# Kernel tuning notes

Hardware: AMD Instinct MI355X
Metric: run time of the kernel (lower is better)

## Reference

```python
import jax, jax.numpy as jnp
import numpy as np

N_NODES = 50000
N_EDGES = 800000
IN_F = 128
HID_F = 128
OUT_F = 128

def safediv(a, b):
    b = jnp.where(b == 0, jnp.ones_like(b), b)
    return a / b

def setup_inputs() -> dict:
    key = jax.random.key(0)
    ks = jax.random.split(key, 8)
    h = jax.random.normal(ks[0], (N_NODES, IN_F), dtype=jnp.float32)
    ppr_weight = jax.random.uniform(ks[1], (N_EDGES,), dtype=jnp.float32)
    Qw = jax.random.normal(ks[2], (HID_F, IN_F), dtype=jnp.float32) * (1.0 / np.sqrt(IN_F))
    Qb = jnp.zeros((HID_F,), dtype=jnp.float32)
    Ww = jax.random.normal(ks[3], (OUT_F, IN_F + HID_F), dtype=jnp.float32) * (1.0 / np.sqrt(IN_F + HID_F))
    Wb = jnp.zeros((OUT_F,), dtype=jnp.float32)
    src = jax.random.randint(ks[4], (N_EDGES,), 0, N_NODES, dtype=jnp.int64 if jax.config.jax_enable_x64 else jnp.int32)
    dst = jax.random.randint(ks[5], (N_EDGES,), 0, N_NODES, dtype=jnp.int64 if jax.config.jax_enable_x64 else jnp.int32)
    return {"h": h, "ppr_weight": ppr_weight, "Qw": Qw, "Qb": Qb, "Ww": Ww, "Wb": Wb, "src": src, "dst": dst}

def reference(h, ppr_weight, Qw, Qb, Ww, Wb, src, dst):
    # neighbor transform: Q(h) -> [N, HID_F]
    hq = h @ Qw.T + Qb
    # message: h_w = hq[src] * ppr_weight  (edge-weighted gather) [E, HID_F]
    msg = hq[src] * ppr_weight[:, None]
    # reduce: scatter-sum messages and weights onto dst nodes
    h_agg = jax.ops.segment_sum(msg, dst, num_segments=N_NODES)
    w = jax.ops.segment_sum(ppr_weight, dst, num_segments=N_NODES)
    # apply: PPR-weighted mean, concat, linear, leaky_relu, L2 normalize
    h_agg = safediv(h_agg, w[:, None])
    h_concat = jnp.concatenate([h, h_agg], axis=1)
    h_new = jax.nn.leaky_relu(h_concat @ Ww.T + Wb, negative_slope=0.01)
    norm = jnp.linalg.norm(h_new, axis=1, keepdims=True)
    return safediv(h_new, norm)
```

## Files before the change

### kernel.cpp

```cpp
#include <hip/hip_runtime.h>
#include <stdint.h>

#define N_NODES 50000
#define N_EDGES 800000
#define IN_F 128
#define HID_F 128
#define OUT_F 128
#define CAT_F 256
#define N_STRIPS 3125

#define NB 256
#define NBUCK 782
#define CHUNK_E (N_EDGES / NB)
#define BCAP 1280

typedef __bf16 bf16x8 __attribute__((ext_vector_type(8)));
typedef float f32x4 __attribute__((ext_vector_type(4)));

union BF8 {
  bf16x8 v;
  uint16_t u[8];
};

__device__ __forceinline__ uint32_t f2b(float f) {
  uint32_t u = __float_as_uint(f);
  return (u + 0x7fffu + ((u >> 16) & 1u)) >> 16;
}

__global__ void __launch_bounds__(256) prep_hist_kernel(
    const int* __restrict__ dst, int* __restrict__ G,
    const float* __restrict__ Qw, const float* __restrict__ Ww,
    uint16_t* __restrict__ QwB, uint16_t* __restrict__ WwB) {
  if (blockIdx.x < NB) {
    __shared__ int hist[NBUCK];
    for (int k = threadIdx.x; k < NBUCK; k += 256) hist[k] = 0;
    __syncthreads();
    int base = blockIdx.x * CHUNK_E;
    for (int e = base + threadIdx.x; e < base + CHUNK_E; e += 256)
      atomicAdd(&hist[dst[e] >> 6], 1);
    __syncthreads();
    for (int k = threadIdx.x; k < NBUCK; k += 256)
      G[k * NB + blockIdx.x] = hist[k];
  } else {
    const int TOT4 = (HID_F * IN_F + OUT_F * CAT_F) / 4;
    int i4 = (blockIdx.x - NB) * 256 + threadIdx.x;
    if (i4 >= TOT4) return;
    int base = i4 * 4;
    const float* src;
    uint16_t* dstp;
    int off;
    if (base < HID_F * IN_F) {
      src = Qw; dstp = QwB; off = base;
    } else {
      src = Ww; dstp = WwB; off = base - HID_F * IN_F;
    }
    float4 v = *(const float4*)(src + off);
    ushort4 o;
    o.x = (uint16_t)f2b(v.x); o.y = (uint16_t)f2b(v.y);
    o.z = (uint16_t)f2b(v.z); o.w = (uint16_t)f2b(v.w);
    *(ushort4*)(dstp + off) = o;
  }
}

__global__ void __launch_bounds__(256) bucket_scan_kernel(const int* __restrict__ G,
                                                          int* __restrict__ Gs,
                                                          int* __restrict__ Btot) {
  int w = (blockIdx.x * 256 + (int)threadIdx.x) >> 6;
  if (w >= NBUCK) return;
  int lane = threadIdx.x & 63;
  int4 v = *(const int4*)(G + (size_t)w * NB + lane * 4);
  int s = v.x + v.y + v.z + v.w;
  int inc = s;
#pragma unroll
  for (int d = 1; d < 64; d <<= 1) {
    int x = __shfl_up(inc, d, 64);
    if (lane >= d) inc += x;
  }
  int exc = inc - s;
  int4 o;
  o.x = exc;
  o.y = exc + v.x;
  o.z = exc + v.x + v.y;
  o.w = exc + v.x + v.y + v.z;
  *(int4*)(Gs + (size_t)w * NB + lane * 4) = o;
  if (lane == 63) Btot[w] = inc;
}

__global__ void base_scan_kernel(const int* __restrict__ Btot, int* __restrict__ Bbase) {
  int lane = threadIdx.x;
  int c[13], loc[13];
  int s = 0;
#pragma unroll
  for (int j = 0; j < 13; ++j) {
    int i = lane * 13 + j;
    c[j] = (i < NBUCK) ? Btot[i] : 0;
    loc[j] = s;
    s += c[j];
  }
  int inc = s;
#pragma unroll
  for (int d = 1; d < 64; d <<= 1) {
    int x = __shfl_up(inc, d, 64);
    if (lane >= d) inc += x;
  }
  int exc = inc - s;
#pragma unroll
  for (int j = 0; j < 13; ++j) {
    int i = lane * 13 + j;
    if (i <= NBUCK) Bbase[i] = exc + loc[j];
  }
}

__device__ __forceinline__ void gemm1_body(int gb, const float* __restrict__ h,
                                           const uint16_t* __restrict__ QwB,
                                           const float* __restrict__ Qb,
                                           uint16_t* __restrict__ hqB) {
  int wave = (gb * 256 + (int)threadIdx.x) >> 6;
  if (wave >= N_STRIPS) return;
  int lane = threadIdx.x & 63;
  int r = lane & 15, qd = lane >> 4;
  int row0 = wave * 16;
  f32x4 acc[8];
#pragma unroll
  for (int t = 0; t < 8; ++t) acc[t] = (f32x4){0.f, 0.f, 0.f, 0.f};
  const float* aRow = h + (size_t)(row0 + r) * IN_F + qd * 8;
#pragma unroll
  for (int kt = 0; kt < 4; ++kt) {
    float4 v0 = *(const float4*)(aRow + kt * 32);
    float4 v1 = *(const float4*)(aRow + kt * 32 + 4);
    BF8 a;
    a.u[0] = (uint16_t)f2b(v0.x); a.u[1] = (uint16_t)f2b(v0.y);
    a.u[2] = (uint16_t)f2b(v0.z); a.u[3] = (uint16_t)f2b(v0.w);
    a.u[4] = (uint16_t)f2b(v1.x); a.u[5] = (uint16_t)f2b(v1.y);
    a.u[6] = (uint16_t)f2b(v1.z); a.u[7] = (uint16_t)f2b(v1.w);
#pragma unroll
    for (int t = 0; t < 8; ++t) {
      bf16x8 b = *(const bf16x8*)(QwB + (t * 16 + r) * IN_F + kt * 32 + qd * 8);
      acc[t] = __builtin_amdgcn_mfma_f32_16x16x32_bf16(a.v, b, acc[t], 0, 0, 0);
    }
  }
#pragma unroll
  for (int t = 0; t < 8; ++t) {
    float qb = Qb[t * 16 + r];
#pragma unroll
    for (int rr = 0; rr < 4; ++rr) {
      int m = row0 + qd * 4 + rr;
      hqB[(size_t)m * HID_F + t * 16 + r] = (uint16_t)f2b(acc[t][rr] + qb);
    }
  }
}

__global__ void __launch_bounds__(256) scatter_gemm1_kernel(
    const int* __restrict__ dst, const int* __restrict__ src, const float* __restrict__ ppr,
    const int* __restrict__ Gs, const int* __restrict__ Bbase, int2* __restrict__ rec,
    const float* __restrict__ h, const uint16_t* __restrict__ QwB,
    const float* __restrict__ Qb, uint16_t* __restrict__ hqB) {
  if (blockIdx.x < NB) {
    __shared__ int cursor[NBUCK];
    int b = blockIdx.x;
    for (int k = threadIdx.x; k < NBUCK; k += 256)
      cursor[k] = Bbase[k] + Gs[(size_t)k * NB + b];
    __syncthreads();
    int base = b * CHUNK_E;
    for (int e = base + threadIdx.x; e < base + CHUNK_E; e += 256) {
      int d = dst[e];
      int s = src[e];
      float w = ppr[e];
      int pos = atomicAdd(&cursor[d >> 6], 1);
      rec[pos] = make_int2(s | ((d & 63) << 20), __float_as_int(w));
    }
  } else {
    gemm1_body(blockIdx.x - NB, h, QwB, Qb, hqB);
  }
}

__global__ void __launch_bounds__(256) agg_gemm2_kernel(
    const uint16_t* __restrict__ hqB, const int2* __restrict__ rec,
    const int* __restrict__ Bbase, const float* __restrict__ h,
    const uint16_t* __restrict__ WwB, const float* __restrict__ Wb,
    float* __restrict__ out) {
  __shared__ int2 srec[BCAP];
  __shared__ uint4 hagg[64][17];
  __shared__ int hist[64];
  __shared__ int noff[65];
  __shared__ int cur[64];
  int g = blockIdx.x;
  int t = threadIdx.x;
  if (t < 64) hist[t] = 0;
  __syncthreads();

  int rbeg = Bbase[g];
  int rend = Bbase[g + 1];
  int len = rend - rbeg;

  for (int i = t; i < len; i += 256) {
    int2 rc = rec[rbeg + i];
    atomicAdd(&hist[rc.x >> 20], 1);
  }
  __syncthreads();

  if (t < 64) {
    int v = hist[t];
    int inc = v;
#pragma unroll
    for (int d = 1; d < 64; d <<= 1) {
      int x = __shfl_up(inc, d, 64);
      if (t >= d) inc += x;
    }
    noff[t] = inc - v;
    cur[t] = inc - v;
    if (t == 63) noff[64] = inc;
  }
  __syncthreads();

  for (int i = t; i < len; i += 256) {
    int2 rc = rec[rbeg + i];
    int p = atomicAdd(&cur[rc.x >> 20], 1);
    if (p < BCAP) srec[p] = rc;
  }
  __syncthreads();

  int lane = t & 63, wv = t >> 6;
  int sub = lane >> 4, c = lane & 15;
  const uint4* hq4 = (const uint4*)hqB;
  for (int nl = wv * 16; nl < wv * 16 + 16; ++nl) {
    int node = g * 64 + nl;
    if (node >= N_NODES) continue;
    int nbeg = noff[nl], nend = noff[nl + 1];
    int m = nend - nbeg;
    float a[8];
#pragma unroll
    for (int j = 0; j < 8; ++j) a[j] = 0.f;
    float ws = 0.f;
    if (m > 0) {
      int last = nend - 1;
      for (int e0 = nbeg; e0 < nend; e0 += 16) {
        int2 rc[4];
#pragma unroll
        for (int q = 0; q < 4; ++q) {
          int i = e0 + q * 4 + sub;
          rc[q] = srec[(i < last) ? i : last];
        }
        uint4 u[4];
#pragma unroll
        for (int q = 0; q < 4; ++q) u[q] = hq4[(size_t)(rc[q].x & 0xFFFFF) * 16 + c];
#pragma unroll
        for (int q = 0; q < 4; ++q) {
          float w = (e0 + q * 4 + sub <= last) ? __int_as_float(rc[q].y) : 0.f;
          ws += w;
          uint32_t x;
          x = u[q].x;
          a[0] += w * __uint_as_float(x << 16);
          a[1] += w * __uint_as_float(x & 0xffff0000u);
          x = u[q].y;
          a[2] += w * __uint_as_float(x << 16);
          a[3] += w * __uint_as_float(x & 0xffff0000u);
          x = u[q].z;
          a[4] += w * __uint_as_float(x << 16);
          a[5] += w * __uint_as_float(x & 0xffff0000u);
          x = u[q].w;
          a[6] += w * __uint_as_float(x << 16);
          a[7] += w * __uint_as_float(x & 0xffff0000u);
        }
      }
    }
#pragma unroll
    for (int j = 0; j < 8; ++j) {
      a[j] += __shfl_xor(a[j], 16);
      a[j] += __shfl_xor(a[j], 32);
    }
    ws += __shfl_xor(ws, 16);
    ws += __shfl_xor(ws, 32);
    float dnm = (ws == 0.f) ? 1.f : ws;
    float inv = 1.f / dnm;
    if (sub == 0) {
      uint4 o;
      o.x = f2b(a[0] * inv) | (f2b(a[1] * inv) << 16);
      o.y = f2b(a[2] * inv) | (f2b(a[3] * inv) << 16);
      o.z = f2b(a[4] * inv) | (f2b(a[5] * inv) << 16);
      o.w = f2b(a[6] * inv) | (f2b(a[7] * inv) << 16);
      hagg[nl][c] = o;
    }
  }
  __syncthreads();

  int row0 = g * 64 + wv * 16;
  if (row0 >= N_NODES) return;
  int r = lane & 15, qd = lane >> 4;
  f32x4 acc[8];
#pragma unroll
  for (int tt = 0; tt < 8; ++tt) acc[tt] = (f32x4){0.f, 0.f, 0.f, 0.f};
  const float* aRow = h + (size_t)(row0 + r) * IN_F + qd * 8;
#pragma unroll
  for (int kt = 0; kt < 8; ++kt) {
    bf16x8 av;
    if (kt < 4) {
      float4 v0 = *(const float4*)(aRow + kt * 32);
      float4 v1 = *(const float4*)(aRow + kt * 32 + 4);
      BF8 ab;
      ab.u[0] = (uint16_t)f2b(v0.x); ab.u[1] = (uint16_t)f2b(v0.y);
      ab.u[2] = (uint16_t)f2b(v0.z); ab.u[3] = (uint16_t)f2b(v0.w);
      ab.u[4] = (uint16_t)f2b(v1.x); ab.u[5] = (uint16_t)f2b(v1.y);
      ab.u[6] = (uint16_t)f2b(v1.z); ab.u[7] = (uint16_t)f2b(v1.w);
      av = ab.v;
    } else {
      av = *(const bf16x8*)&hagg[wv * 16 + r][(kt - 4) * 4 + qd];
    }
#pragma unroll
    for (int tt = 0; tt < 8; ++tt) {
      bf16x8 b = *(const bf16x8*)(WwB + (tt * 16 + r) * CAT_F + kt * 32 + qd * 8);
      acc[tt] = __builtin_amdgcn_mfma_f32_16x16x32_bf16(av, b, acc[tt], 0, 0, 0);
    }
  }
  float lv[8][4];
  float ss[4] = {0.f, 0.f, 0.f, 0.f};
#pragma unroll
  for (int tt = 0; tt < 8; ++tt) {
    float wb = Wb[tt * 16 + r];
#pragma unroll
    for (int rr = 0; rr < 4; ++rr) {
      float v = acc[tt][rr] + wb;
      v = (v >= 0.f) ? v : 0.01f * v;
      lv[tt][rr] = v;
      ss[rr] += v * v;
    }
  }
#pragma unroll
  for (int rr = 0; rr < 4; ++rr) {
    float s = ss[rr];
    s += __shfl_xor(s, 1);
    s += __shfl_xor(s, 2);
    s += __shfl_xor(s, 4);
    s += __shfl_xor(s, 8);
    float nr = sqrtf(s);
    float inv = (nr == 0.f) ? 1.f : (1.f / nr);
    int mrow = row0 + qd * 4 + rr;
    float* orow = out + (size_t)mrow * OUT_F;
#pragma unroll
    for (int tt = 0; tt < 8; ++tt) orow[tt * 16 + r] = lv[tt][rr] * inv;
  }
}

extern "C" void kernel_launch(void* const* d_in, const int* in_sizes, int n_in,
                              void* d_out, int out_size, void* d_ws, size_t ws_size,
                              hipStream_t stream) {
  const float* h = (const float*)d_in[0];
  const float* ppr = (const float*)d_in[1];
  const float* Qw = (const float*)d_in[2];
  const float* Qb = (const float*)d_in[3];
  const float* Ww = (const float*)d_in[4];
  const float* Wb = (const float*)d_in[5];
  const int* src = (const int*)d_in[6];
  const int* dst = (const int*)d_in[7];
  float* out = (float*)d_out;

  char* ws = (char*)d_ws;
  size_t o = 0;
  auto alloc = [&](size_t bytes) {
    void* p = ws + o;
    o = (o + bytes + 255) & ~(size_t)255;
    return p;
  };
  uint16_t* hqB = (uint16_t*)alloc((size_t)N_NODES * HID_F * 2);
  uint16_t* QwB = (uint16_t*)alloc((size_t)HID_F * IN_F * 2);
  uint16_t* WwB = (uint16_t*)alloc((size_t)OUT_F * CAT_F * 2);
  int* G = (int*)alloc((size_t)NBUCK * NB * 4);
  int* Gs = (int*)alloc((size_t)NBUCK * NB * 4);
  int* Btot = (int*)alloc((size_t)NBUCK * 4);
  int* Bbase = (int*)alloc((size_t)(NBUCK + 1) * 4);
  int2* rec = (int2*)alloc((size_t)N_EDGES * 8);

  prep_hist_kernel<<<NB + 48, 256, 0, stream>>>(dst, G, Qw, Ww, QwB, WwB);
  bucket_scan_kernel<<<(NBUCK + 3) / 4, 256, 0, stream>>>(G, Gs, Btot);
  base_scan_kernel<<<1, 64, 0, stream>>>(Btot, Bbase);
  scatter_gemm1_kernel<<<NB + 782, 256, 0, stream>>>(dst, src, ppr, Gs, Bbase, rec, h, QwB,
                                                     Qb, hqB);
  agg_gemm2_kernel<<<NBUCK, 256, 0, stream>>>(hqB, rec, Bbase, h, WwB, Wb, out);
}
```

Baseline: 190.3 us.

## Halve dst buckets, precast h to bf16, vectorize edge loads, one-node-per-subwave aggregation

Buckets shrink from 64 to 32 nodes (1563 buckets, 128-thread aggregation blocks), and the edge histogram and scatter read dst/src/ppr as int4/float4. h is converted once to bf16 in the prep kernel, so both GEMMs load bf16 directly. Aggregation now gives each 16-lane subgroup its own node instead of splitting one node across the wave, and records are kept in registers between the two passes. The cost is an extra h conversion pass and more blocks. Per-bucket records are now truncated at BCAP=640, which silently drops edges if a bucket overflows.

```diff
diff --git a/kernel.cpp b/kernel.cpp
--- a/kernel.cpp
+++ b/kernel.cpp
@@ -10,17 +10,12 @@
 #define N_STRIPS 3125
 
 #define NB 256
-#define NBUCK 782
-#define CHUNK_E (N_EDGES / NB)
-#define BCAP 1280
+#define CHUNK 3136
+#define NBUCK 1563
+#define BCAP 640
 
 typedef __bf16 bf16x8 __attribute__((ext_vector_type(8)));
 typedef float f32x4 __attribute__((ext_vector_type(4)));
-
-union BF8 {
-  bf16x8 v;
-  uint16_t u[8];
-};
 
 __device__ __forceinline__ uint32_t f2b(float f) {
   uint32_t u = __float_as_uint(f);
@@ -28,31 +23,39 @@
 }
 
 __global__ void __launch_bounds__(256) prep_hist_kernel(
-    const int* __restrict__ dst, int* __restrict__ G,
-    const float* __restrict__ Qw, const float* __restrict__ Ww,
+    const int* __restrict__ dst, int* __restrict__ G, const float* __restrict__ h,
+    const float* __restrict__ Qw, const float* __restrict__ Ww, uint16_t* __restrict__ hB,
     uint16_t* __restrict__ QwB, uint16_t* __restrict__ WwB) {
   if (blockIdx.x < NB) {
     __shared__ int hist[NBUCK];
     for (int k = threadIdx.x; k < NBUCK; k += 256) hist[k] = 0;
     __syncthreads();
-    int base = blockIdx.x * CHUNK_E;
-    for (int e = base + threadIdx.x; e < base + CHUNK_E; e += 256)
-      atomicAdd(&hist[dst[e] >> 6], 1);
+    int b = blockIdx.x;
+    int base = b * CHUNK;
+    int end = (base + CHUNK < N_EDGES) ? (base + CHUNK) : N_EDGES;
+    for (int i4 = base / 4 + threadIdx.x; i4 * 4 < end; i4 += 256) {
+      int4 d4 = ((const int4*)dst)[i4];
+      atomicAdd(&hist[d4.x >> 5], 1);
+      atomicAdd(&hist[d4.y >> 5], 1);
+      atomicAdd(&hist[d4.z >> 5], 1);
+      atomicAdd(&hist[d4.w >> 5], 1);
+    }
     __syncthreads();
-    for (int k = threadIdx.x; k < NBUCK; k += 256)
-      G[k * NB + blockIdx.x] = hist[k];
+    for (int k = threadIdx.x; k < NBUCK; k += 256) G[k * NB + b] = hist[k];
   } else {
-    const int TOT4 = (HID_F * IN_F + OUT_F * CAT_F) / 4;
+    const int TOT4 = (N_NODES * IN_F + HID_F * IN_F + OUT_F * CAT_F) / 4;
     int i4 = (blockIdx.x - NB) * 256 + threadIdx.x;
     if (i4 >= TOT4) return;
     int base = i4 * 4;
     const float* src;
     uint16_t* dstp;
     int off;
-    if (base < HID_F * IN_F) {
-      src = Qw; dstp = QwB; off = base;
+    if (base < N_NODES * IN_F) {
+      src = h; dstp = hB; off = base;
+    } else if (base < N_NODES * IN_F + HID_F * IN_F) {
+      src = Qw; dstp = QwB; off = base - N_NODES * IN_F;
     } else {
-      src = Ww; dstp = WwB; off = base - HID_F * IN_F;
+      src = Ww; dstp = WwB; off = base - N_NODES * IN_F - HID_F * IN_F;
     }
     float4 v = *(const float4*)(src + off);
     ushort4 o;
@@ -88,11 +91,11 @@
 
 __global__ void base_scan_kernel(const int* __restrict__ Btot, int* __restrict__ Bbase) {
   int lane = threadIdx.x;
-  int c[13], loc[13];
+  int c[25], loc[25];
   int s = 0;
 #pragma unroll
-  for (int j = 0; j < 13; ++j) {
-    int i = lane * 13 + j;
+  for (int j = 0; j < 25; ++j) {
+    int i = lane * 25 + j;
     c[j] = (i < NBUCK) ? Btot[i] : 0;
     loc[j] = s;
     s += c[j];
@@ -105,13 +108,13 @@
   }
   int exc = inc - s;
 #pragma unroll
-  for (int j = 0; j < 13; ++j) {
-    int i = lane * 13 + j;
+  for (int j = 0; j < 25; ++j) {
+    int i = lane * 25 + j;
     if (i <= NBUCK) Bbase[i] = exc + loc[j];
   }
 }
 
-__device__ __forceinline__ void gemm1_body(int gb, const float* __restrict__ h,
+__device__ __forceinline__ void gemm1_body(int gb, const uint16_t* __restrict__ hB,
                                            const uint16_t* __restrict__ QwB,
                                            const float* __restrict__ Qb,
                                            uint16_t* __restrict__ hqB) {
@@ -123,20 +126,14 @@
   f32x4 acc[8];
 #pragma unroll
   for (int t = 0; t < 8; ++t) acc[t] = (f32x4){0.f, 0.f, 0.f, 0.f};
-  const float* aRow = h + (size_t)(row0 + r) * IN_F + qd * 8;
+  const uint16_t* aRow = hB + (size_t)(row0 + r) * IN_F + qd * 8;
 #pragma unroll
   for (int kt = 0; kt < 4; ++kt) {
-    float4 v0 = *(const float4*)(aRow + kt * 32);
-    float4 v1 = *(const float4*)(aRow + kt * 32 + 4);
-    BF8 a;
-    a.u[0] = (uint16_t)f2b(v0.x); a.u[1] = (uint16_t)f2b(v0.y);
-    a.u[2] = (uint16_t)f2b(v0.z); a.u[3] = (uint16_t)f2b(v0.w);
-    a.u[4] = (uint16_t)f2b(v1.x); a.u[5] = (uint16_t)f2b(v1.y);
-    a.u[6] = (uint16_t)f2b(v1.z); a.u[7] = (uint16_t)f2b(v1.w);
+    bf16x8 a = *(const bf16x8*)(aRow + kt * 32);
 #pragma unroll
     for (int t = 0; t < 8; ++t) {
       bf16x8 b = *(const bf16x8*)(QwB + (t * 16 + r) * IN_F + kt * 32 + qd * 8);
-      acc[t] = __builtin_amdgcn_mfma_f32_16x16x32_bf16(a.v, b, acc[t], 0, 0, 0);
+      acc[t] = __builtin_amdgcn_mfma_f32_16x16x32_bf16(a, b, acc[t], 0, 0, 0);
     }
   }
 #pragma unroll
@@ -153,7 +150,7 @@
 __global__ void __launch_bounds__(256) scatter_gemm1_kernel(
     const int* __restrict__ dst, const int* __restrict__ src, const float* __restrict__ ppr,
     const int* __restrict__ Gs, const int* __restrict__ Bbase, int2* __restrict__ rec,
-    const float* __restrict__ h, const uint16_t* __restrict__ QwB,
+    const uint16_t* __restrict__ hB, const uint16_t* __restrict__ QwB,
     const float* __restrict__ Qb, uint16_t* __restrict__ hqB) {
   if (blockIdx.x < NB) {
     __shared__ int cursor[NBUCK];
@@ -161,119 +158,126 @@
     for (int k = threadIdx.x; k < NBUCK; k += 256)
       cursor[k] = Bbase[k] + Gs[(size_t)k * NB + b];
     __syncthreads();
-    int base = b * CHUNK_E;
-    for (int e = base + threadIdx.x; e < base + CHUNK_E; e += 256) {
-      int d = dst[e];
-      int s = src[e];
-      float w = ppr[e];
-      int pos = atomicAdd(&cursor[d >> 6], 1);
-      rec[pos] = make_int2(s | ((d & 63) << 20), __float_as_int(w));
+    int base = b * CHUNK;
+    int end = (base + CHUNK < N_EDGES) ? (base + CHUNK) : N_EDGES;
+    for (int i4 = base / 4 + threadIdx.x; i4 * 4 < end; i4 += 256) {
+      int4 d4 = ((const int4*)dst)[i4];
+      int4 s4 = ((const int4*)src)[i4];
+      float4 w4 = ((const float4*)ppr)[i4];
+      int p;
+      p = atomicAdd(&cursor[d4.x >> 5], 1);
+      rec[p] = make_int2(s4.x | ((d4.x & 31) << 20), __float_as_int(w4.x));
+      p = atomicAdd(&cursor[d4.y >> 5], 1);
+      rec[p] = make_int2(s4.y | ((d4.y & 31) << 20), __float_as_int(w4.y));
+      p = atomicAdd(&cursor[d4.z >> 5], 1);
+      rec[p] = make_int2(s4.z | ((d4.z & 31) << 20), __float_as_int(w4.z));
+      p = atomicAdd(&cursor[d4.w >> 5], 1);
+      rec[p] = make_int2(s4.w | ((d4.w & 31) << 20), __float_as_int(w4.w));
     }
   } else {
-    gemm1_body(blockIdx.x - NB, h, QwB, Qb, hqB);
-  }
-}
-
-__global__ void __launch_bounds__(256) agg_gemm2_kernel(
+    gemm1_body(blockIdx.x - NB, hB, QwB, Qb, hqB);
+  }
+}
+
+__global__ void __launch_bounds__(128) agg_gemm2_kernel(
     const uint16_t* __restrict__ hqB, const int2* __restrict__ rec,
-    const int* __restrict__ Bbase, const float* __restrict__ h,
+    const int* __restrict__ Bbase, const uint16_t* __restrict__ hB,
     const uint16_t* __restrict__ WwB, const float* __restrict__ Wb,
     float* __restrict__ out) {
   __shared__ int2 srec[BCAP];
-  __shared__ uint4 hagg[64][17];
-  __shared__ int hist[64];
-  __shared__ int noff[65];
-  __shared__ int cur[64];
+  __shared__ uint4 hagg[32][17];
+  __shared__ int hist[32];
+  __shared__ int noff[33];
+  __shared__ int cur[32];
   int g = blockIdx.x;
   int t = threadIdx.x;
-  if (t < 64) hist[t] = 0;
+  if (t < 32) hist[t] = 0;
   __syncthreads();
 
   int rbeg = Bbase[g];
-  int rend = Bbase[g + 1];
-  int len = rend - rbeg;
-
-  for (int i = t; i < len; i += 256) {
-    int2 rc = rec[rbeg + i];
-    atomicAdd(&hist[rc.x >> 20], 1);
-  }
-  __syncthreads();
-
-  if (t < 64) {
+  int len = Bbase[g + 1] - rbeg;
+  len = (len < BCAP) ? len : BCAP;
+
+  int2 rc[5];
+#pragma unroll
+  for (int k = 0; k < 5; ++k) {
+    int i = t + k * 128;
+    if (i < len) {
+      rc[k] = rec[rbeg + i];
+      atomicAdd(&hist[rc[k].x >> 20], 1);
+    }
+  }
+  __syncthreads();
+
+  if (t < 32) {
     int v = hist[t];
     int inc = v;
 #pragma unroll
-    for (int d = 1; d < 64; d <<= 1) {
+    for (int d = 1; d < 32; d <<= 1) {
       int x = __shfl_up(inc, d, 64);
       if (t >= d) inc += x;
     }
     noff[t] = inc - v;
     cur[t] = inc - v;
-    if (t == 63) noff[64] = inc;
-  }
-  __syncthreads();
-
-  for (int i = t; i < len; i += 256) {
-    int2 rc = rec[rbeg + i];
-    int p = atomicAdd(&cur[rc.x >> 20], 1);
-    if (p < BCAP) srec[p] = rc;
+    if (t == 31) noff[32] = inc;
+  }
+  __syncthreads();
+
+#pragma unroll
+  for (int k = 0; k < 5; ++k) {
+    int i = t + k * 128;
+    if (i < len) {
+      int p = atomicAdd(&cur[rc[k].x >> 20], 1);
+      srec[p] = rc[k];
+    }
   }
   __syncthreads();
 
   int lane = t & 63, wv = t >> 6;
   int sub = lane >> 4, c = lane & 15;
   const uint4* hq4 = (const uint4*)hqB;
-  for (int nl = wv * 16; nl < wv * 16 + 16; ++nl) {
-    int node = g * 64 + nl;
-    if (node >= N_NODES) continue;
-    int nbeg = noff[nl], nend = noff[nl + 1];
-    int m = nend - nbeg;
-    float a[8];
-#pragma unroll
-    for (int j = 0; j < 8; ++j) a[j] = 0.f;
-    float ws = 0.f;
-    if (m > 0) {
-      int last = nend - 1;
-      for (int e0 = nbeg; e0 < nend; e0 += 16) {
-        int2 rc[4];
-#pragma unroll
-        for (int q = 0; q < 4; ++q) {
-          int i = e0 + q * 4 + sub;
-          rc[q] = srec[(i < last) ? i : last];
+#pragma unroll
+  for (int g4 = 0; g4 < 4; ++g4) {
+    int nl = wv * 16 + g4 * 4 + sub;
+    int node = g * 32 + nl;
+    if (node < N_NODES) {
+      int nbeg = noff[nl], nend = noff[nl + 1];
+      float a[8];
+#pragma unroll
+      for (int j = 0; j < 8; ++j) a[j] = 0.f;
+      float ws = 0.f;
+      for (int e0 = nbeg; e0 < nend; e0 += 4) {
+        int last = nend - 1;
+        int2 rr[4];
+#pragma unroll
+        for (int j = 0; j < 4; ++j) {
+          int i = e0 + j;
+          rr[j] = srec[(i < last) ? i : last];
         }
         uint4 u[4];
 #pragma unroll
-        for (int q = 0; q < 4; ++q) u[q] = hq4[(size_t)(rc[q].x & 0xFFFFF) * 16 + c];
-#pragma unroll
-        for (int q = 0; q < 4; ++q) {
-          float w = (e0 + q * 4 + sub <= last) ? __int_as_float(rc[q].y) : 0.f;
+        for (int j = 0; j < 4; ++j) u[j] = hq4[(size_t)(rr[j].x & 0xFFFFF) * 16 + c];
+#pragma unroll
+        for (int j = 0; j < 4; ++j) {
+          float w = (e0 + j < nend) ? __int_as_float(rr[j].y) : 0.f;
           ws += w;
           uint32_t x;
-          x = u[q].x;
+          x = u[j].x;
           a[0] += w * __uint_as_float(x << 16);
           a[1] += w * __uint_as_float(x & 0xffff0000u);
-          x = u[q].y;
+          x = u[j].y;
           a[2] += w * __uint_as_float(x << 16);
           a[3] += w * __uint_as_float(x & 0xffff0000u);
-          x = u[q].z;
+          x = u[j].z;
           a[4] += w * __uint_as_float(x << 16);
           a[5] += w * __uint_as_float(x & 0xffff0000u);
-          x = u[q].w;
+          x = u[j].w;
           a[6] += w * __uint_as_float(x << 16);
           a[7] += w * __uint_as_float(x & 0xffff0000u);
         }
       }
-    }
-#pragma unroll
-    for (int j = 0; j < 8; ++j) {
-      a[j] += __shfl_xor(a[j], 16);
-      a[j] += __shfl_xor(a[j], 32);
-    }
-    ws += __shfl_xor(ws, 16);
-    ws += __shfl_xor(ws, 32);
-    float dnm = (ws == 0.f) ? 1.f : ws;
-    float inv = 1.f / dnm;
-    if (sub == 0) {
+      float dnm = (ws == 0.f) ? 1.f : ws;
+      float inv = 1.f / dnm;
       uint4 o;
       o.x = f2b(a[0] * inv) | (f2b(a[1] * inv) << 16);
       o.y = f2b(a[2] * inv) | (f2b(a[3] * inv) << 16);
@@ -284,25 +288,18 @@
   }
   __syncthreads();
 
-  int row0 = g * 64 + wv * 16;
+  int row0 = g * 32 + wv * 16;
   if (row0 >= N_NODES) return;
   int r = lane & 15, qd = lane >> 4;
   f32x4 acc[8];
 #pragma unroll
   for (int tt = 0; tt < 8; ++tt) acc[tt] = (f32x4){0.f, 0.f, 0.f, 0.f};
-  const float* aRow = h + (size_t)(row0 + r) * IN_F + qd * 8;
+  const uint16_t* aRow = hB + (size_t)(row0 + r) * IN_F + qd * 8;
 #pragma unroll
   for (int kt = 0; kt < 8; ++kt) {
     bf16x8 av;
     if (kt < 4) {
-      float4 v0 = *(const float4*)(aRow + kt * 32);
-      float4 v1 = *(const float4*)(aRow + kt * 32 + 4);
-      BF8 ab;
-      ab.u[0] = (uint16_t)f2b(v0.x); ab.u[1] = (uint16_t)f2b(v0.y);
-      ab.u[2] = (uint16_t)f2b(v0.z); ab.u[3] = (uint16_t)f2b(v0.w);
-      ab.u[4] = (uint16_t)f2b(v1.x); ab.u[5] = (uint16_t)f2b(v1.y);
-      ab.u[6] = (uint16_t)f2b(v1.z); ab.u[7] = (uint16_t)f2b(v1.w);
-      av = ab.v;
+      av = *(const bf16x8*)(aRow + kt * 32);
     } else {
       av = *(const bf16x8*)&hagg[wv * 16 + r][(kt - 4) * 4 + qd];
     }
@@ -318,26 +315,26 @@
   for (int tt = 0; tt < 8; ++tt) {
     float wb = Wb[tt * 16 + r];
 #pragma unroll
-    for (int rr = 0; rr < 4; ++rr) {
-      float v = acc[tt][rr] + wb;
+    for (int rr2 = 0; rr2 < 4; ++rr2) {
+      float v = acc[tt][rr2] + wb;
       v = (v >= 0.f) ? v : 0.01f * v;
-      lv[tt][rr] = v;
-      ss[rr] += v * v;
-    }
-  }
-#pragma unroll
-  for (int rr = 0; rr < 4; ++rr) {
-    float s = ss[rr];
+      lv[tt][rr2] = v;
+      ss[rr2] += v * v;
+    }
+  }
+#pragma unroll
+  for (int rr2 = 0; rr2 < 4; ++rr2) {
+    float s = ss[rr2];
     s += __shfl_xor(s, 1);
     s += __shfl_xor(s, 2);
     s += __shfl_xor(s, 4);
     s += __shfl_xor(s, 8);
     float nr = sqrtf(s);
     float inv = (nr == 0.f) ? 1.f : (1.f / nr);
-    int mrow = row0 + qd * 4 + rr;
+    int mrow = row0 + qd * 4 + rr2;
     float* orow = out + (size_t)mrow * OUT_F;
 #pragma unroll
-    for (int tt = 0; tt < 8; ++tt) orow[tt * 16 + r] = lv[tt][rr] * inv;
+    for (int tt = 0; tt < 8; ++tt) orow[tt * 16 + r] = lv[tt][rr2] * inv;
   }
 }
 
@@ -361,6 +358,7 @@
     o = (o + bytes + 255) & ~(size_t)255;
     return p;
   };
+  uint16_t* hB = (uint16_t*)alloc((size_t)N_NODES * IN_F * 2);
   uint16_t* hqB = (uint16_t*)alloc((size_t)N_NODES * HID_F * 2);
   uint16_t* QwB = (uint16_t*)alloc((size_t)HID_F * IN_F * 2);
   uint16_t* WwB = (uint16_t*)alloc((size_t)OUT_F * CAT_F * 2);
@@ -370,10 +368,11 @@
   int* Bbase = (int*)alloc((size_t)(NBUCK + 1) * 4);
   int2* rec = (int2*)alloc((size_t)N_EDGES * 8);
 
-  prep_hist_kernel<<<NB + 48, 256, 0, stream>>>(dst, G, Qw, Ww, QwB, WwB);
+  const int CONV_BLOCKS = ((N_NODES * IN_F + HID_F * IN_F + OUT_F * CAT_F) / 4 + 255) / 256;
+  prep_hist_kernel<<<NB + CONV_BLOCKS, 256, 0, stream>>>(dst, G, h, Qw, Ww, hB, QwB, WwB);
   bucket_scan_kernel<<<(NBUCK + 3) / 4, 256, 0, stream>>>(G, Gs, Btot);
   base_scan_kernel<<<1, 64, 0, stream>>>(Btot, Bbase);
-  scatter_gemm1_kernel<<<NB + 782, 256, 0, stream>>>(dst, src, ppr, Gs, Bbase, rec, h, QwB,
+  scatter_gemm1_kernel<<<NB + 782, 256, 0, stream>>>(dst, src, ppr, Gs, Bbase, rec, hB, QwB,
                                                      Qb, hqB);
-  agg_gemm2_kernel<<<NBUCK, 256, 0, stream>>>(hqB, rec, Bbase, h, WwB, Wb, out);
-}
+  agg_gemm2_kernel<<<NBUCK, 128, 0, stream>>>(hqB, rec, Bbase, hB, WwB, Wb, out);
+}
```

Measured after the change: 179.8 us. -5.5%, faster.
